# Kernel tuning notes

Measured on AMD Instinct MI355X. Metric: run time of the kernel, lower is better.

The kernel has to match this reference:

```python
import jax, jax.numpy as jnp
import numpy as np
import math

EPS = 1e-6
N_NODES = 25000
N_EDGES = 400000
F = 8            # multivector channels
NB = 8           # blades of Cl(3,0)
NORM_FACTOR = 1.0
SUBSPACES = np.array([1, 3, 3, 1])
REP = np.repeat(np.arange(4), SUBSPACES)   # grade index per blade: [0,1,1,1,2,2,2,3]
GRADES = np.array([0, 1, 1, 1, 2, 2, 2, 3])

def _build_cayley():
    # shortlex blade order for dim 3: 1, e1, e2, e3, e12, e13, e23, e123
    bitmaps = [0, 1, 2, 4, 3, 5, 6, 7]
    b2i = {b: i for i, b in enumerate(bitmaps)}
    def sign(a, b):
        a >>= 1
        s = 0
        while a:
            s += bin(a & b).count('1')
            a >>= 1
        return 1.0 if s % 2 == 0 else -1.0  # euclidean metric (1,1,1)
    C = np.zeros((NB, NB, NB), np.float32)
    for i, bi in enumerate(bitmaps):
        for j, bj in enumerate(bitmaps):
            C[i, b2i[bi ^ bj], j] = sign(bi, bj)   # cayley[left, out, right]
    return C

CAYLEY_NP = _build_cayley()

def _paths():
    p = np.zeros((4, 4, 4), bool)
    for a in range(4):
        for b in range(4):
            for c in range(4):
                blk = CAYLEY_NP[GRADES == a][:, GRADES == b][:, :, GRADES == c]
                p[a, b, c] = np.any(blk != 0)
    return np.nonzero(p)

PI, PJ, PK = _paths()
N_PATHS = len(PI)  # 20 for Cl(3,0)
CAYLEY = jnp.asarray(CAYLEY_NP)

def grade_qs(x):
    # per-grade quadratic form (euclidean: sum of squares), x: [..., 8] -> [..., 4]
    sq = x * x
    return jnp.concatenate([sq[..., 0:1],
                            sq[..., 1:4].sum(-1, keepdims=True),
                            sq[..., 4:7].sum(-1, keepdims=True),
                            sq[..., 7:8]], axis=-1)

def mv_linear(x, w, b=None):
    # w: [out, in, 4] grade-wise weights, repeat-interleaved over blades
    out = jnp.einsum('bmi,nmi->bni', x, w[:, :, REP])
    if b is not None:
        out = out.at[:, :, 0].add(b[0, :, 0])   # bias embedded in scalar blade
    return out

def mv_silu(x, a, b):
    q = grade_qs(x)
    inv = jnp.concatenate([x[..., :1], q[..., 1:]], axis=-1)  # scalar + mag2 per grade
    gate = jax.nn.sigmoid(a * inv + b)[..., REP]
    return gate * x

def sgp(x, w_right, w_geo, w_left, b_left, a_norm):
    # SteerableGeometricProductLayer with NormalizationLayer on the right input
    xr = mv_linear(x, w_right)
    norms = jnp.sqrt(grade_qs(xr))                       # [B,F,4]
    norms = jax.nn.sigmoid(a_norm) * (norms - 1.0) + 1.0
    xr = xr / (norms[..., REP] + EPS)
    W4 = jnp.zeros((F, 4, 4, 4), x.dtype).at[:, PI, PJ, PK].set(w_geo)
    W8 = W4[:, REP][:, :, REP][:, :, :, REP] * CAYLEY    # [F,8,8,8]
    geo = jnp.einsum('bni,nijk,bnk->bnj', x, W8, xr)
    return (mv_linear(x, w_left, b_left) + geo) / math.sqrt(2.0)

def mv_layernorm(x, a):
    n = jnp.sqrt((x * x).sum(-1, keepdims=True)).mean(axis=1, keepdims=True) + EPS
    return a[..., None] * x / n

def block(x, lin_w, lin_b, silu_a, silu_b, gp_wr, gp_w, gp_wl, gp_bl, gp_an, ln_a):
    # CEMLP block: MVLinear -> MVSiLU -> SteerableGeometricProduct -> MVLayerNorm
    x = mv_linear(x, lin_w, lin_b)
    x = mv_silu(x, silu_a, silu_b)
    x = sgp(x, gp_wr, gp_w, gp_wl, gp_bl, gp_an)
    return mv_layernorm(x, ln_a)

def setup_inputs() -> dict:
    key = jax.random.key(0)
    ks = jax.random.split(key, 12)
    h = jax.random.normal(ks[0], (N_NODES, F, NB), jnp.float32)
    edge_index = jax.random.randint(ks[1], (2, N_EDGES), 0, N_NODES)
    def linw(k, out_f, in_f):
        return jax.random.normal(k, (out_f, in_f, 4), jnp.float32) / math.sqrt(in_f)
    inp = dict(h=h, edge_index=edge_index)
    for pref, kk in (('e', 2), ('n', 7)):
        inp[pref + '_lin_w'] = linw(ks[kk], F, 2 * F)
        inp[pref + '_lin_b'] = jnp.zeros((1, F, 1), jnp.float32)
        inp[pref + '_silu_a'] = jnp.ones((1, F, 4), jnp.float32)
        inp[pref + '_silu_b'] = jnp.zeros((1, F, 4), jnp.float32)
        inp[pref + '_gp_wr'] = linw(ks[kk + 1], F, F)
        inp[pref + '_gp_w'] = jax.random.normal(ks[kk + 2], (F, N_PATHS), jnp.float32) / 2.0
        inp[pref + '_gp_wl'] = linw(ks[kk + 3], F, F)
        inp[pref + '_gp_bl'] = jnp.zeros((1, F, 1), jnp.float32)
        inp[pref + '_gp_an'] = jnp.zeros((F, 4), jnp.float32)
        inp[pref + '_ln_a'] = jnp.ones((1, F), jnp.float32)
    return inp

def reference(h, edge_index,
              e_lin_w, e_lin_b, e_silu_a, e_silu_b, e_gp_wr, e_gp_w, e_gp_wl, e_gp_bl, e_gp_an, e_ln_a,
              n_lin_w, n_lin_b, n_silu_a, n_silu_b, n_gp_wr, n_gp_w, n_gp_wl, n_gp_bl, n_gp_an, n_ln_a):
    row, col = edge_index[0], edge_index[1]
    # edge model: gather endpoint features, Clifford MLP block
    m = jnp.concatenate([h[row], h[col]], axis=1)          # [E, 2F, 8]
    m = block(m, e_lin_w, e_lin_b, e_silu_a, e_silu_b,
              e_gp_wr, e_gp_w, e_gp_wl, e_gp_bl, e_gp_an, e_ln_a)
    # unsorted_segment_sum on flattened multivectors, 'sum' aggregation
    agg = jax.ops.segment_sum(m.reshape(N_EDGES, -1), row, num_segments=N_NODES) / NORM_FACTOR
    agg = agg.reshape(N_NODES, F, NB)
    # node update: residual Clifford MLP block on [h, agg]
    upd = jnp.concatenate([h, agg], axis=1)                # [N, 2F, 8]
    upd = block(upd, n_lin_w, n_lin_b, n_silu_a, n_silu_b,
                n_gp_wr, n_gp_w, n_gp_wl, n_gp_bl, n_gp_an, n_ln_a)
    return h + upd
```

## Files before the change

### kernel.cpp

```cpp
#include <hip/hip_runtime.h>

#define NNODES 25000
#define NEDGES 400000
#define EPB 32
#define XSTR2 68
#define EPSF 1e-6f
#define RSQRT2 0.7071067811865476f

typedef _Float16 half8 __attribute__((ext_vector_type(8)));

static constexpr int GJ[64] = {
 0,1,2,3,4,5,6,7,
 1,0,4,5,2,3,7,6,
 2,4,0,6,1,7,3,5,
 3,5,6,0,7,1,2,4,
 4,2,1,7,0,6,5,3,
 5,3,7,1,6,0,4,2,
 6,7,3,2,5,4,0,1,
 7,6,5,4,3,2,1,0};
static constexpr int GS[64] = {
 1, 1, 1, 1, 1, 1, 1, 1,
 1, 1, 1, 1, 1, 1, 1, 1,
 1,-1, 1, 1,-1,-1, 1,-1,
 1,-1,-1, 1, 1,-1,-1, 1,
 1,-1, 1, 1,-1,-1, 1,-1,
 1,-1,-1, 1, 1,-1,-1, 1,
 1, 1,-1, 1,-1, 1,-1,-1,
 1, 1,-1, 1,-1, 1,-1,-1};
static constexpr int GP[64] = {
  0, 1, 1, 1, 2, 2, 2, 3,
  5, 4, 7, 7, 6, 6, 9, 8,
  5, 7, 4, 7, 6, 9, 6, 8,
  5, 7, 7, 4, 9, 6, 6, 8,
 13,11,11,15,10,14,14,12,
 13,11,15,11,14,10,14,12,
 13,15,11,11,14,14,10,12,
 19,18,18,18,17,17,17,16};

struct WP {
  const float *wlin, *blin, *asi, *bsi, *wr, *wg, *wl, *bl, *an, *aln;
};

__device__ __forceinline__ float sigm(float x) {
  return __builtin_amdgcn_rcpf(1.f + __expf(-x));
}
__device__ __forceinline__ float frcp(float x) { return __builtin_amdgcn_rcpf(x); }
__device__ __forceinline__ float fsqrt(float x) { return __builtin_amdgcn_sqrtf(x); }

__device__ __forceinline__ void wave_fence() {
  asm volatile("s_waitcnt lgkmcnt(0)" ::: "memory");
  __builtin_amdgcn_sched_barrier(0);
}

#define C_WR   0
#define C_WL   (C_WR + 288)
#define C_WG   (C_WL + 288)
#define C_BLIN (C_WG + 160)
#define C_ASI  (C_BLIN + 8)
#define C_BSI  (C_ASI + 32)
#define C_BL   (C_BSI + 32)
#define C_AN   (C_BL + 8)
#define C_ALN  (C_AN + 32)
#define C_TOT  (C_ALN + 8)
#define C_WLIN C_TOT
#define CN_TOT (C_WLIN + 8*68)

__device__ __forceinline__ void stage_common(int tid, float* Ws, const WP& wp) {
  int t = tid;
  if (t < 256) Ws[C_WR + (t >> 5) * 36 + (t & 31)] = wp.wr[t];
  if (t < 256) Ws[C_WL + (t >> 5) * 36 + (t & 31)] = wp.wl[t];
  if (t < 160) Ws[C_WG + t] = wp.wg[t];
  if (t < 8)   Ws[C_BLIN + t] = wp.blin[t];
  if (t < 32)  Ws[C_ASI + t] = wp.asi[t];
  if (t < 32)  Ws[C_BSI + t] = wp.bsi[t];
  if (t < 8)   Ws[C_BL + t]  = wp.bl[t];
  if (t < 32)  Ws[C_AN + t]  = wp.an[t];
  if (t < 8)   Ws[C_ALN + t] = wp.aln[t];
}

__device__ __forceinline__ void clifford_tail(float* __restrict__ X,
                                              const float* __restrict__ Ws,
                                              int n, const float* y, float* z)
{
  const float q1 = y[1]*y[1] + y[2]*y[2] + y[3]*y[3];
  const float q2 = y[4]*y[4] + y[5]*y[5] + y[6]*y[6];
  const float q3 = y[7]*y[7];
  const float g0 = sigm(Ws[C_ASI + n*4 + 0] * y[0] + Ws[C_BSI + n*4 + 0]);
  const float g1 = sigm(Ws[C_ASI + n*4 + 1] * q1  + Ws[C_BSI + n*4 + 1]);
  const float g2 = sigm(Ws[C_ASI + n*4 + 2] * q2  + Ws[C_BSI + n*4 + 2]);
  const float g3 = sigm(Ws[C_ASI + n*4 + 3] * q3  + Ws[C_BSI + n*4 + 3]);
  float s[8] = { g0*y[0], g1*y[1], g1*y[2], g1*y[3],
                 g2*y[4], g2*y[5], g2*y[6], g3*y[7] };
  *(float4*)&X[n*8]     = make_float4(s[0], s[1], s[2], s[3]);
  *(float4*)&X[n*8 + 4] = make_float4(s[4], s[5], s[6], s[7]);
  wave_fence();

  float xr[8], zl[8];
  #pragma unroll
  for (int i = 0; i < 8; ++i) { xr[i] = 0.f; zl[i] = 0.f; }
  #pragma unroll
  for (int m = 0; m < 8; ++m) {
    const float4 wr4 = *(const float4*)&Ws[C_WR + n * 36 + m * 4];
    const float4 wl4 = *(const float4*)&Ws[C_WL + n * 36 + m * 4];
    const float4 xa = *(const float4*)&X[m * 8];
    const float4 xb = *(const float4*)&X[m * 8 + 4];
    xr[0]=fmaf(xa.x,wr4.x,xr[0]); xr[1]=fmaf(xa.y,wr4.y,xr[1]); xr[2]=fmaf(xa.z,wr4.y,xr[2]); xr[3]=fmaf(xa.w,wr4.y,xr[3]);
    xr[4]=fmaf(xb.x,wr4.z,xr[4]); xr[5]=fmaf(xb.y,wr4.z,xr[5]); xr[6]=fmaf(xb.z,wr4.z,xr[6]); xr[7]=fmaf(xb.w,wr4.w,xr[7]);
    zl[0]=fmaf(xa.x,wl4.x,zl[0]); zl[1]=fmaf(xa.y,wl4.y,zl[1]); zl[2]=fmaf(xa.z,wl4.y,zl[2]); zl[3]=fmaf(xa.w,wl4.y,zl[3]);
    zl[4]=fmaf(xb.x,wl4.z,zl[4]); zl[5]=fmaf(xb.y,wl4.z,zl[5]); zl[6]=fmaf(xb.z,wl4.z,zl[6]); zl[7]=fmaf(xb.w,wl4.w,zl[7]);
  }
  zl[0] += Ws[C_BL + n];

  {
    const float t0 = fabsf(xr[0]);
    const float t1 = fsqrt(xr[1]*xr[1] + xr[2]*xr[2] + xr[3]*xr[3]);
    const float t2 = fsqrt(xr[4]*xr[4] + xr[5]*xr[5] + xr[6]*xr[6]);
    const float t3 = fabsf(xr[7]);
    const float d0 = frcp(sigm(Ws[C_AN + n*4 + 0]) * (t0 - 1.f) + 1.f + EPSF);
    const float d1 = frcp(sigm(Ws[C_AN + n*4 + 1]) * (t1 - 1.f) + 1.f + EPSF);
    const float d2 = frcp(sigm(Ws[C_AN + n*4 + 2]) * (t2 - 1.f) + 1.f + EPSF);
    const float d3 = frcp(sigm(Ws[C_AN + n*4 + 3]) * (t3 - 1.f) + 1.f + EPSF);
    xr[0] *= d0; xr[1] *= d1; xr[2] *= d1; xr[3] *= d1;
    xr[4] *= d2; xr[5] *= d2; xr[6] *= d2; xr[7] *= d3;
  }

  float geo[8];
  #pragma unroll
  for (int i = 0; i < 8; ++i) geo[i] = 0.f;
  {
    const int wgb = C_WG + n * 20;
    #pragma unroll
    for (int i = 0; i < 8; ++i) {
      #pragma unroll
      for (int k = 0; k < 8; ++k) {
        const float t = s[i] * xr[k];
        const float w = Ws[wgb + GP[i * 8 + k]];
        geo[GJ[i * 8 + k]] = fmaf(GS[i * 8 + k] > 0 ? w : -w, t, geo[GJ[i * 8 + k]]);
      }
    }
  }

  #pragma unroll
  for (int i = 0; i < 8; ++i) z[i] = (zl[i] + geo[i]) * RSQRT2;

  float sq = 0.f;
  #pragma unroll
  for (int i = 0; i < 8; ++i) sq = fmaf(z[i], z[i], sq);
  float nr = fsqrt(sq);
  nr += __shfl_xor(nr, 1);
  nr += __shfl_xor(nr, 2);
  nr += __shfl_xor(nr, 4);
  const float scale = Ws[C_ALN + n] * frcp(nr * 0.125f + EPSF);
  #pragma unroll
  for (int i = 0; i < 8; ++i) z[i] *= scale;
}

__global__ __launch_bounds__(1024)
void csr_scan_fast(const int* __restrict__ deg, int* __restrict__ ptr,
                   int* __restrict__ fill)
{
  __shared__ int wsum[16];
  const int t = threadIdx.x;
  const int base = t * 32;
  int d[32];
  int s = 0;
  #pragma unroll
  for (int i = 0; i < 8; ++i) {
    int idx = base + i * 4;
    int4 v = make_int4(0, 0, 0, 0);
    if (idx + 3 < NNODES) v = *(const int4*)(deg + idx);
    else {
      if (idx + 0 < NNODES) v.x = deg[idx + 0];
      if (idx + 1 < NNODES) v.y = deg[idx + 1];
      if (idx + 2 < NNODES) v.z = deg[idx + 2];
    }
    d[i*4+0] = v.x; d[i*4+1] = v.y; d[i*4+2] = v.z; d[i*4+3] = v.w;
    s += v.x + v.y + v.z + v.w;
  }
  const int lane = t & 63;
  int incl = s;
  #pragma unroll
  for (int off = 1; off < 64; off <<= 1) {
    int u = __shfl_up(incl, off);
    if (lane >= off) incl += u;
  }
  const int wv = t >> 6;
  if (lane == 63) wsum[wv] = incl;
  __syncthreads();
  if (t < 16) {
    int v = wsum[t];
    int inc = v;
    #pragma unroll
    for (int off = 1; off < 16; off <<= 1) {
      int u = __shfl_up(inc, off);
      if (t >= off) inc += u;
    }
    wsum[t] = inc - v;
  }
  __syncthreads();
  int run = wsum[wv] + (incl - s);
  #pragma unroll
  for (int i = 0; i < 8; ++i) {
    int idx = base + i * 4;
    int4 pv;
    pv.x = run; run += d[i*4+0];
    pv.y = run; run += d[i*4+1];
    pv.z = run; run += d[i*4+2];
    pv.w = run; run += d[i*4+3];
    if (idx + 3 < NNODES) {
      *(int4*)(ptr + idx)  = pv;
      *(int4*)(fill + idx) = pv;
    } else {
      if (idx + 0 < NNODES) { ptr[idx+0] = pv.x; fill[idx+0] = pv.x; }
      if (idx + 1 < NNODES) { ptr[idx+1] = pv.y; fill[idx+1] = pv.y; }
      if (idx + 2 < NNODES) { ptr[idx+2] = pv.z; fill[idx+2] = pv.z; }
    }
  }
  if (t == 1023) ptr[NNODES] = NEDGES;
}

#define PRE_BLOCKS ((NNODES + EPB - 1) / EPB)
#define CNT_BLOCKS ((NEDGES + 255) / 256)

__global__ __launch_bounds__(256)
void pre_count(const float* __restrict__ h,
               const float* __restrict__ wle,
               float* __restrict__ ue, float* __restrict__ ve,
               const int* __restrict__ eidx, int* __restrict__ deg)
{
  __shared__ __align__(16) float We[8 * 68];
  __shared__ __align__(16) float Xs[EPB * XSTR2];
  const int tid = threadIdx.x;

  if (blockIdx.x >= PRE_BLOCKS) {
    int e = (blockIdx.x - PRE_BLOCKS) * 256 + tid;
    if (e < NEDGES) atomicAdd(&deg[eidx[e]], 1);
    return;
  }

  for (int t = tid; t < 512; t += 256) We[(t >> 6) * 68 + (t & 63)] = wle[t];
  const int el = tid >> 3, n = tid & 7;
  const int item = blockIdx.x * EPB + el;
  float* X = &Xs[el * XSTR2];
  const bool act = item < NNODES;
  if (act) {
    const float4* ph = (const float4*)(h + (size_t)item * 64 + n * 8);
    *(float4*)&X[n * 8]     = ph[0];
    *(float4*)&X[n * 8 + 4] = ph[1];
  }
  __syncthreads();
  if (!act) return;
  float ua[8], va[8];
  #pragma unroll
  for (int i = 0; i < 8; ++i) { ua[i] = 0.f; va[i] = 0.f; }
  #pragma unroll
  for (int m = 0; m < 8; ++m) {
    const float4 xa = *(const float4*)&X[m * 8];
    const float4 xb = *(const float4*)&X[m * 8 + 4];
    const float4 wa = *(const float4*)&We[n * 68 + m * 4];
    const float4 wb = *(const float4*)&We[n * 68 + (m + 8) * 4];
    ua[0]=fmaf(xa.x,wa.x,ua[0]); ua[1]=fmaf(xa.y,wa.y,ua[1]); ua[2]=fmaf(xa.z,wa.y,ua[2]); ua[3]=fmaf(xa.w,wa.y,ua[3]);
    ua[4]=fmaf(xb.x,wa.z,ua[4]); ua[5]=fmaf(xb.y,wa.z,ua[5]); ua[6]=fmaf(xb.z,wa.z,ua[6]); ua[7]=fmaf(xb.w,wa.w,ua[7]);
    va[0]=fmaf(xa.x,wb.x,va[0]); va[1]=fmaf(xa.y,wb.y,va[1]); va[2]=fmaf(xa.z,wb.y,va[2]); va[3]=fmaf(xa.w,wb.y,va[3]);
    va[4]=fmaf(xb.x,wb.z,va[4]); va[5]=fmaf(xb.y,wb.z,va[5]); va[6]=fmaf(xb.z,wb.z,va[6]); va[7]=fmaf(xb.w,wb.w,va[7]);
  }
  float4* pu = (float4*)(ue + (size_t)item * 64 + n * 8);
  pu[0] = make_float4(ua[0],ua[1],ua[2],ua[3]); pu[1] = make_float4(ua[4],ua[5],ua[6],ua[7]);
  float4* pv = (float4*)(ve + (size_t)item * 64 + n * 8);
  pv[0] = make_float4(va[0],va[1],va[2],va[3]); pv[1] = make_float4(va[4],va[5],va[6],va[7]);
}

__global__ __launch_bounds__(256) void csr_scatter_pairs(const int* __restrict__ eidx,
                                                         int* __restrict__ fill,
                                                         int2* __restrict__ ers) {
  int e = blockIdx.x * 256 + threadIdx.x;
  if (e < NEDGES) {
    const int r = eidx[e];
    const int c = eidx[NEDGES + e];
    int pos = atomicAdd(&fill[r], 1);
    ers[pos] = make_int2(r, c);
  }
}

__global__ __launch_bounds__(256)
void cgenn5_edge(const int2* __restrict__ ers,
                 const float* __restrict__ ue, const float* __restrict__ ve,
                 _Float16* __restrict__ msgh, WP wp)
{
  __shared__ __align__(16) float Ws[C_TOT];
  __shared__ __align__(16) float Xs[EPB * XSTR2];
  const int tid = threadIdx.x;
  const int el = tid >> 3, n = tid & 7;
  const int p = blockIdx.x * EPB + el;

  const int2 rc = ers[p];
  const float4* pu = (const float4*)(ue + (size_t)rc.x * 64 + n * 8);
  const float4 u0 = pu[0], u1 = pu[1];
  const float4* pv = (const float4*)(ve + (size_t)rc.y * 64 + n * 8);
  const float4 v0 = pv[0], v1 = pv[1];

  stage_common(tid, Ws, wp);
  __syncthreads();

  float y[8] = { u0.x+v0.x, u0.y+v0.y, u0.z+v0.z, u0.w+v0.w,
                 u1.x+v1.x, u1.y+v1.y, u1.z+v1.z, u1.w+v1.w };
  y[0] += Ws[C_BLIN + n];

  float z[8];
  clifford_tail(&Xs[el * XSTR2], Ws, n, y, z);

  half8 hm;
  hm[0]=(_Float16)z[0]; hm[1]=(_Float16)z[1]; hm[2]=(_Float16)z[2]; hm[3]=(_Float16)z[3];
  hm[4]=(_Float16)z[4]; hm[5]=(_Float16)z[5]; hm[6]=(_Float16)z[6]; hm[7]=(_Float16)z[7];
  *(half8*)(msgh + (size_t)p * 64 + n * 8) = hm;
}

#define NPB 4
__global__ __launch_bounds__(256)
void cgenn5_node(const float* __restrict__ h,
                 const _Float16* __restrict__ msgh,
                 const int* __restrict__ ptr,
                 float* __restrict__ out, WP wp)
{
  __shared__ __align__(16) float Ws[CN_TOT];
  __shared__ __align__(16) float Xs[NPB * 132];
  const int tid  = threadIdx.x;
  const int wv   = tid >> 6;
  const int slot = (tid >> 3) & 7;
  const int n    = tid & 7;
  const int nid  = blockIdx.x * NPB + wv;
  float* X = &Xs[wv * 132];

  stage_common(tid, Ws, wp);
  for (int t = tid; t < 512; t += 256)
    Ws[C_WLIN + (t >> 6) * 68 + (t & 63)] = wp.wlin[t];

  const int beg = ptr[nid], end = ptr[nid + 1];

  float a[8];
  #pragma unroll
  for (int i = 0; i < 8; ++i) a[i] = 0.f;
  const _Float16* mb = msgh + (size_t)n * 8;
  for (int p = beg + slot; p < end; p += 8) {
    const half8 m = *(const half8*)(mb + (size_t)p * 64);
    #pragma unroll
    for (int i = 0; i < 8; ++i) a[i] += (float)m[i];
  }
  #pragma unroll
  for (int i = 0; i < 8; ++i) {
    a[i] += __shfl_xor(a[i], 8);
    a[i] += __shfl_xor(a[i], 16);
    a[i] += __shfl_xor(a[i], 32);
  }

  __syncthreads();

  if (slot == 0) {
    float hr[8];
    const float4* ph = (const float4*)(h + (size_t)nid * 64 + n * 8);
    const float4 h0 = ph[0], h1 = ph[1];
    hr[0]=h0.x; hr[1]=h0.y; hr[2]=h0.z; hr[3]=h0.w;
    hr[4]=h1.x; hr[5]=h1.y; hr[6]=h1.z; hr[7]=h1.w;
    *(float4*)&X[n*8]         = h0;
    *(float4*)&X[n*8 + 4]     = h1;
    *(float4*)&X[(8+n)*8]     = make_float4(a[0], a[1], a[2], a[3]);
    *(float4*)&X[(8+n)*8 + 4] = make_float4(a[4], a[5], a[6], a[7]);
    wave_fence();

    float y[8];
    #pragma unroll
    for (int i = 0; i < 8; ++i) y[i] = 0.f;
    #pragma unroll
    for (int m = 0; m < 16; ++m) {
      const float4 w4 = *(const float4*)&Ws[C_WLIN + n * 68 + m * 4];
      const float4 xa = *(const float4*)&X[m * 8];
      const float4 xb = *(const float4*)&X[m * 8 + 4];
      y[0]=fmaf(xa.x,w4.x,y[0]); y[1]=fmaf(xa.y,w4.y,y[1]); y[2]=fmaf(xa.z,w4.y,y[2]); y[3]=fmaf(xa.w,w4.y,y[3]);
      y[4]=fmaf(xb.x,w4.z,y[4]); y[5]=fmaf(xb.y,w4.z,y[5]); y[6]=fmaf(xb.z,w4.z,y[6]); y[7]=fmaf(xb.w,w4.w,y[7]);
    }
    y[0] += Ws[C_BLIN + n];

    float z[8];
    clifford_tail(X, Ws, n, y, z);

    float4* po = (float4*)(out + (size_t)nid * 64 + n * 8);
    po[0] = make_float4(hr[0]+z[0], hr[1]+z[1], hr[2]+z[2], hr[3]+z[3]);
    po[1] = make_float4(hr[4]+z[4], hr[5]+z[5], hr[6]+z[6], hr[7]+z[7]);
  }
}

template<bool IS_NODE>
__global__ __launch_bounds__(256)
void cgenn_block(const float* __restrict__ h,
                 const int* __restrict__ eidx,
                 float* agg_out, WP wp)
{
  __shared__ __align__(16) float Ws[CN_TOT];
  __shared__ __align__(16) float Xs[EPB * 132];
  const int tid = threadIdx.x;
  stage_common(tid, Ws, wp);
  for (int t = tid; t < 512; t += 256)
    Ws[C_WLIN + (t >> 6) * 68 + (t & 63)] = wp.wlin[t];
  const int el = tid >> 3;
  const int n  = tid & 7;
  const int item = blockIdx.x * EPB + el;
  float* X = &Xs[el * 132];
  bool active = true;
  int r = 0;
  float hr[8];
  if (IS_NODE) {
    active = (item < NNODES);
    if (active) {
      const float4* ph = (const float4*)(h + (size_t)item * 64 + n * 8);
      float4 a0 = ph[0], a1 = ph[1];
      hr[0]=a0.x; hr[1]=a0.y; hr[2]=a0.z; hr[3]=a0.w;
      hr[4]=a1.x; hr[5]=a1.y; hr[6]=a1.z; hr[7]=a1.w;
      *(float4*)&X[n*8]     = a0;
      *(float4*)&X[n*8 + 4] = a1;
      const float4* pa = (const float4*)(agg_out + (size_t)item * 64 + n * 8);
      *(float4*)&X[(8+n)*8]     = pa[0];
      *(float4*)&X[(8+n)*8 + 4] = pa[1];
    }
  } else {
    r = eidx[item];
    const int c = eidx[NEDGES + item];
    const float4* ph = (const float4*)(h + (size_t)r * 64 + n * 8);
    float4 a0 = ph[0], a1 = ph[1];
    const float4* pc = (const float4*)(h + (size_t)c * 64 + n * 8);
    float4 b0 = pc[0], b1 = pc[1];
    *(float4*)&X[n*8]       = a0;  *(float4*)&X[n*8 + 4]     = a1;
    *(float4*)&X[(8+n)*8]   = b0;  *(float4*)&X[(8+n)*8 + 4] = b1;
  }
  __syncthreads();
  float y[8];
  #pragma unroll
  for (int i = 0; i < 8; ++i) y[i] = 0.f;
  #pragma unroll
  for (int m = 0; m < 16; ++m) {
    const float4 w4 = *(const float4*)&Ws[C_WLIN + n * 68 + m * 4];
    const float4 xa = *(const float4*)&X[m * 8];
    const float4 xb = *(const float4*)&X[m * 8 + 4];
    y[0]=fmaf(xa.x,w4.x,y[0]); y[1]=fmaf(xa.y,w4.y,y[1]); y[2]=fmaf(xa.z,w4.y,y[2]); y[3]=fmaf(xa.w,w4.y,y[3]);
    y[4]=fmaf(xb.x,w4.z,y[4]); y[5]=fmaf(xb.y,w4.z,y[5]); y[6]=fmaf(xb.z,w4.z,y[6]); y[7]=fmaf(xb.w,w4.w,y[7]);
  }
  y[0] += Ws[C_BLIN + n];
  float z[8];
  clifford_tail(X, Ws, n, y, z);
  if (IS_NODE) {
    if (active) {
      float4* po = (float4*)(agg_out + (size_t)item * 64 + n * 8);
      po[0] = make_float4(hr[0]+z[0], hr[1]+z[1], hr[2]+z[2], hr[3]+z[3]);
      po[1] = make_float4(hr[4]+z[4], hr[5]+z[5], hr[6]+z[6], hr[7]+z[7]);
    }
  } else {
    float* dst = agg_out + (size_t)r * 64 + n * 8;
    #pragma unroll
    for (int i = 0; i < 8; ++i) atomicAdd(dst + i, z[i]);
  }
}

extern "C" void kernel_launch(void* const* d_in, const int* in_sizes, int n_in,
                              void* d_out, int out_size, void* d_ws, size_t ws_size,
                              hipStream_t stream)
{
  (void)in_sizes; (void)n_in; (void)out_size;
  const float* h   = (const float*)d_in[0];
  const int* eidx  = (const int*)d_in[1];
  WP we = { (const float*)d_in[2],  (const float*)d_in[3],  (const float*)d_in[4],
            (const float*)d_in[5],  (const float*)d_in[6],  (const float*)d_in[7],
            (const float*)d_in[8],  (const float*)d_in[9],  (const float*)d_in[10],
            (const float*)d_in[11] };
  WP wn = { (const float*)d_in[12], (const float*)d_in[13], (const float*)d_in[14],
            (const float*)d_in[15], (const float*)d_in[16], (const float*)d_in[17],
            (const float*)d_in[18], (const float*)d_in[19], (const float*)d_in[20],
            (const float*)d_in[21] };
  float* out = (float*)d_out;

  const size_t mhsz   = (size_t)NEDGES * 64 * sizeof(_Float16);
  const size_t nodef  = (size_t)NNODES * 64 * sizeof(float);
  const size_t pairsz = (size_t)NEDGES * sizeof(int2);
  const size_t degsz  = (size_t)25008 * sizeof(int);
  const size_t fillsz = (size_t)25008 * sizeof(int);
  const size_t need   = mhsz + 2 * nodef + pairsz + degsz + fillsz;

  if (ws_size >= need) {
    char* base = (char*)d_ws;
    _Float16* msgh = (_Float16*)base;   base += mhsz;
    float* ue   = (float*)base;         base += nodef;
    float* ve   = (float*)base;         base += nodef;
    int2* ers   = (int2*)base;          base += pairsz;
    int* deg    = (int*)base;           base += degsz;
    int* fill   = (int*)base;

    hipMemsetAsync(deg, 0, (NNODES + 1) * sizeof(int), stream);
    pre_count<<<dim3(PRE_BLOCKS + CNT_BLOCKS), dim3(256), 0, stream>>>(
        h, we.wlin, ue, ve, eidx, deg);
    csr_scan_fast<<<dim3(1), dim3(1024), 0, stream>>>(deg, deg, fill);
    csr_scatter_pairs<<<dim3(CNT_BLOCKS), dim3(256), 0, stream>>>(eidx, fill, ers);
    cgenn5_edge<<<dim3(NEDGES / EPB), dim3(256), 0, stream>>>(ers, ue, ve, msgh, we);
    cgenn5_node<<<dim3(NNODES / NPB), dim3(256), 0, stream>>>(h, msgh, deg, out, wn);
  } else {
    hipMemsetAsync(d_out, 0, (size_t)NNODES * 64 * sizeof(float), stream);
    cgenn_block<false><<<dim3(NEDGES / EPB), dim3(256), 0, stream>>>(h, eidx, out, we);
    cgenn_block<true><<<dim3((NNODES + EPB - 1) / EPB), dim3(256), 0, stream>>>(h, eidx, out, wn);
  }
}
```

Baseline: 153.2 us.

## Fuse edge MLP into node kernel, computing messages per CSR row on the fly

Merges the edge kernel and the node aggregation kernel into one. Each node's wave now walks its own CSR edge list, gathers the neighbour projections, runs the edge Clifford tail and accumulates in registers. This drops the fp16 message buffer write and read and the row-index array, and stages both weight sets in shared memory. In exchange, each wave's edge-loop length follows its node degree, so imbalanced degrees leave lanes idle through the shared rounds, and shared-memory use per block grows.

```diff
diff --git a/kernel.cpp b/kernel.cpp
--- a/kernel.cpp
+++ b/kernel.cpp
@@ -6,8 +6,6 @@
 #define XSTR2 68
 #define EPSF 1e-6f
 #define RSQRT2 0.7071067811865476f
-
-typedef _Float16 half8 __attribute__((ext_vector_type(8)));
 
 static constexpr int GJ[64] = {
  0,1,2,3,4,5,6,7,
@@ -270,82 +268,74 @@
   pv[0] = make_float4(va[0],va[1],va[2],va[3]); pv[1] = make_float4(va[4],va[5],va[6],va[7]);
 }
 
-__global__ __launch_bounds__(256) void csr_scatter_pairs(const int* __restrict__ eidx,
-                                                         int* __restrict__ fill,
-                                                         int2* __restrict__ ers) {
+__global__ __launch_bounds__(256) void csr_scatter_cols(const int* __restrict__ eidx,
+                                                        int* __restrict__ fill,
+                                                        int* __restrict__ cols) {
   int e = blockIdx.x * 256 + threadIdx.x;
   if (e < NEDGES) {
     const int r = eidx[e];
     const int c = eidx[NEDGES + e];
     int pos = atomicAdd(&fill[r], 1);
-    ers[pos] = make_int2(r, c);
-  }
-}
-
-__global__ __launch_bounds__(256)
-void cgenn5_edge(const int2* __restrict__ ers,
-                 const float* __restrict__ ue, const float* __restrict__ ve,
-                 _Float16* __restrict__ msgh, WP wp)
-{
-  __shared__ __align__(16) float Ws[C_TOT];
-  __shared__ __align__(16) float Xs[EPB * XSTR2];
-  const int tid = threadIdx.x;
-  const int el = tid >> 3, n = tid & 7;
-  const int p = blockIdx.x * EPB + el;
-
-  const int2 rc = ers[p];
-  const float4* pu = (const float4*)(ue + (size_t)rc.x * 64 + n * 8);
-  const float4 u0 = pu[0], u1 = pu[1];
-  const float4* pv = (const float4*)(ve + (size_t)rc.y * 64 + n * 8);
-  const float4 v0 = pv[0], v1 = pv[1];
-
-  stage_common(tid, Ws, wp);
-  __syncthreads();
-
-  float y[8] = { u0.x+v0.x, u0.y+v0.y, u0.z+v0.z, u0.w+v0.w,
-                 u1.x+v1.x, u1.y+v1.y, u1.z+v1.z, u1.w+v1.w };
-  y[0] += Ws[C_BLIN + n];
-
-  float z[8];
-  clifford_tail(&Xs[el * XSTR2], Ws, n, y, z);
-
-  half8 hm;
-  hm[0]=(_Float16)z[0]; hm[1]=(_Float16)z[1]; hm[2]=(_Float16)z[2]; hm[3]=(_Float16)z[3];
-  hm[4]=(_Float16)z[4]; hm[5]=(_Float16)z[5]; hm[6]=(_Float16)z[6]; hm[7]=(_Float16)z[7];
-  *(half8*)(msgh + (size_t)p * 64 + n * 8) = hm;
+    cols[pos] = c;
+  }
 }
 
 #define NPB 4
 __global__ __launch_bounds__(256)
-void cgenn5_node(const float* __restrict__ h,
-                 const _Float16* __restrict__ msgh,
-                 const int* __restrict__ ptr,
-                 float* __restrict__ out, WP wp)
-{
-  __shared__ __align__(16) float Ws[CN_TOT];
-  __shared__ __align__(16) float Xs[NPB * 132];
+void cgenn6_fused(const float* __restrict__ h,
+                  const float* __restrict__ ue, const float* __restrict__ ve,
+                  const int* __restrict__ ptr, const int* __restrict__ cols,
+                  float* __restrict__ out, WP we, WP wn)
+{
+  __shared__ __align__(16) float Ws[C_TOT + CN_TOT];
+  __shared__ __align__(16) float Xe[NPB * 8 * 68];
+  __shared__ __align__(16) float Xn[NPB * 132];
   const int tid  = threadIdx.x;
   const int wv   = tid >> 6;
   const int slot = (tid >> 3) & 7;
   const int n    = tid & 7;
   const int nid  = blockIdx.x * NPB + wv;
-  float* X = &Xs[wv * 132];
-
-  stage_common(tid, Ws, wp);
+
+  stage_common(tid, Ws, we);
+  stage_common(tid, Ws + C_TOT, wn);
   for (int t = tid; t < 512; t += 256)
-    Ws[C_WLIN + (t >> 6) * 68 + (t & 63)] = wp.wlin[t];
+    Ws[C_TOT + C_WLIN + (t >> 6) * 68 + (t & 63)] = wn.wlin[t];
 
   const int beg = ptr[nid], end = ptr[nid + 1];
 
+  const float4* pu = (const float4*)(ue + (size_t)nid * 64 + n * 8);
+  const float4 u0 = pu[0], u1 = pu[1];
+
+  __syncthreads();
+
+  const float eb = Ws[C_BLIN + n];
+  float* Xg = &Xe[(wv * 8 + slot) * 68];
+
   float a[8];
   #pragma unroll
   for (int i = 0; i < 8; ++i) a[i] = 0.f;
-  const _Float16* mb = msgh + (size_t)n * 8;
-  for (int p = beg + slot; p < end; p += 8) {
-    const half8 m = *(const half8*)(mb + (size_t)p * 64);
-    #pragma unroll
-    for (int i = 0; i < 8; ++i) a[i] += (float)m[i];
-  }
+
+  const int rounds = (end - beg + 7) >> 3;
+  for (int rd = 0; rd < rounds; ++rd) {
+    const int p = beg + rd * 8 + slot;
+    const bool act = (p < end);
+    float4 v0 = make_float4(0.f, 0.f, 0.f, 0.f);
+    float4 v1 = v0;
+    if (act) {
+      const int c = cols[p];
+      const float4* pv = (const float4*)(ve + (size_t)c * 64 + n * 8);
+      v0 = pv[0]; v1 = pv[1];
+    }
+    float y[8] = { u0.x+v0.x + eb, u0.y+v0.y, u0.z+v0.z, u0.w+v0.w,
+                   u1.x+v1.x, u1.y+v1.y, u1.z+v1.z, u1.w+v1.w };
+    float z[8];
+    clifford_tail(Xg, Ws, n, y, z);
+    if (act) {
+      #pragma unroll
+      for (int i = 0; i < 8; ++i) a[i] += z[i];
+    }
+  }
+
   #pragma unroll
   for (int i = 0; i < 8; ++i) {
     a[i] += __shfl_xor(a[i], 8);
@@ -353,9 +343,9 @@
     a[i] += __shfl_xor(a[i], 32);
   }
 
-  __syncthreads();
-
   if (slot == 0) {
+    const float* Wn = Ws + C_TOT;
+    float* X = &Xn[wv * 132];
     float hr[8];
     const float4* ph = (const float4*)(h + (size_t)nid * 64 + n * 8);
     const float4 h0 = ph[0], h1 = ph[1];
@@ -372,16 +362,16 @@
     for (int i = 0; i < 8; ++i) y[i] = 0.f;
     #pragma unroll
     for (int m = 0; m < 16; ++m) {
-      const float4 w4 = *(const float4*)&Ws[C_WLIN + n * 68 + m * 4];
+      const float4 w4 = *(const float4*)&Wn[C_WLIN + n * 68 + m * 4];
       const float4 xa = *(const float4*)&X[m * 8];
       const float4 xb = *(const float4*)&X[m * 8 + 4];
       y[0]=fmaf(xa.x,w4.x,y[0]); y[1]=fmaf(xa.y,w4.y,y[1]); y[2]=fmaf(xa.z,w4.y,y[2]); y[3]=fmaf(xa.w,w4.y,y[3]);
       y[4]=fmaf(xb.x,w4.z,y[4]); y[5]=fmaf(xb.y,w4.z,y[5]); y[6]=fmaf(xb.z,w4.z,y[6]); y[7]=fmaf(xb.w,w4.w,y[7]);
     }
-    y[0] += Ws[C_BLIN + n];
+    y[0] += Wn[C_BLIN + n];
 
     float z[8];
-    clifford_tail(X, Ws, n, y, z);
+    clifford_tail(X, Wn, n, y, z);
 
     float4* po = (float4*)(out + (size_t)nid * 64 + n * 8);
     po[0] = make_float4(hr[0]+z[0], hr[1]+z[1], hr[2]+z[2], hr[3]+z[3]);
@@ -476,19 +466,17 @@
             (const float*)d_in[21] };
   float* out = (float*)d_out;
 
-  const size_t mhsz   = (size_t)NEDGES * 64 * sizeof(_Float16);
   const size_t nodef  = (size_t)NNODES * 64 * sizeof(float);
-  const size_t pairsz = (size_t)NEDGES * sizeof(int2);
+  const size_t colsz  = (size_t)NEDGES * sizeof(int);
   const size_t degsz  = (size_t)25008 * sizeof(int);
   const size_t fillsz = (size_t)25008 * sizeof(int);
-  const size_t need   = mhsz + 2 * nodef + pairsz + degsz + fillsz;
+  const size_t need   = 2 * nodef + colsz + degsz + fillsz;
 
   if (ws_size >= need) {
     char* base = (char*)d_ws;
-    _Float16* msgh = (_Float16*)base;   base += mhsz;
     float* ue   = (float*)base;         base += nodef;
     float* ve   = (float*)base;         base += nodef;
-    int2* ers   = (int2*)base;          base += pairsz;
+    int* cols   = (int*)base;           base += colsz;
     int* deg    = (int*)base;           base += degsz;
     int* fill   = (int*)base;
 
@@ -496,9 +484,9 @@
     pre_count<<<dim3(PRE_BLOCKS + CNT_BLOCKS), dim3(256), 0, stream>>>(
         h, we.wlin, ue, ve, eidx, deg);
     csr_scan_fast<<<dim3(1), dim3(1024), 0, stream>>>(deg, deg, fill);
-    csr_scatter_pairs<<<dim3(CNT_BLOCKS), dim3(256), 0, stream>>>(eidx, fill, ers);
-    cgenn5_edge<<<dim3(NEDGES / EPB), dim3(256), 0, stream>>>(ers, ue, ve, msgh, we);
-    cgenn5_node<<<dim3(NNODES / NPB), dim3(256), 0, stream>>>(h, msgh, deg, out, wn);
+    csr_scatter_cols<<<dim3(CNT_BLOCKS), dim3(256), 0, stream>>>(eidx, fill, cols);
+    cgenn6_fused<<<dim3(NNODES / NPB), dim3(256), 0, stream>>>(
+        h, ue, ve, deg, cols, out, we, wn);
   } else {
     hipMemsetAsync(d_out, 0, (size_t)NNODES * 64 * sizeof(float), stream);
     cgenn_block<false><<<dim3(NEDGES / EPB), dim3(256), 0, stream>>>(h, eidx, out, we);
```

Measured after the change: 173.6 us. 13.3% more time.
